# Performance work log

Measured on AMD Instinct MI355X. Metric: run time of the kernel, lower is better.

The kernel has to match this reference:

```python
import jax, jax.numpy as jnp
import numpy as np

N_NODES = 400_000
N_EDGES = 1_600_000
F_IN = 100          # len(nonterminals)
EMB = 128           # opts.embedding_dim
SORTK = 64          # opts.sortk
G = 11              # 1 goal graph + 10 local-context graphs (classifier_1 = Linear(11*dense_dim,...))
D_CAT = 3 * EMB + 1 # concat of x1,x2,x3,x4
K5 = 3 * EMB + 1    # conv5 kernel == stride
DENSE_DIM = ((SORTK - 2) // 2 + 1 - 5 + 1) * EMB  # 28*128 = 3584


def setup_inputs() -> dict:
    key = jax.random.key(0)
    ks = jax.random.split(key, 16)
    s = 0.05
    inp = {
        "x": jax.random.normal(ks[0], (N_NODES, F_IN), jnp.float32),
        "edge_index": jax.random.randint(ks[1], (2, N_EDGES), 0, N_NODES, jnp.int64 if jax.config.jax_enable_x64 else jnp.int32),
        "batch": jnp.sort(jax.random.randint(ks[2], (N_NODES,), 0, G)),
        # GCNConv weights (PyG: x @ W + b after propagation)
        "W1": jax.random.normal(ks[3], (F_IN, EMB), jnp.float32) * s,
        "b1": jnp.zeros((EMB,), jnp.float32),
        "W2": jax.random.normal(ks[4], (EMB, EMB), jnp.float32) * s,
        "b2": jnp.zeros((EMB,), jnp.float32),
        "W3": jax.random.normal(ks[5], (EMB, EMB), jnp.float32) * s,
        "b3": jnp.zeros((EMB,), jnp.float32),
        "W4": jax.random.normal(ks[6], (EMB, 1), jnp.float32) * s,
        "b4": jnp.zeros((1,), jnp.float32),
        # Conv1d(1, EMB//2, K5, stride=K5)
        "cw5": jax.random.normal(ks[7], (EMB // 2, 1, K5), jnp.float32) * s,
        "cb5": jnp.zeros((EMB // 2,), jnp.float32),
        # Conv1d(EMB//2, EMB, 5, stride=1)
        "cw6": jax.random.normal(ks[8], (EMB, EMB // 2, 5), jnp.float32) * s,
        "cb6": jnp.zeros((EMB,), jnp.float32),
        # Linear(11*dense_dim, 128), Linear(128, 10)
        "fw1": jax.random.normal(ks[9], (128, G * DENSE_DIM), jnp.float32) * s,
        "fb1": jnp.zeros((128,), jnp.float32),
        "fw2": jax.random.normal(ks[10], (10, 128), jnp.float32) * s,
        "fb2": jnp.zeros((10,), jnp.float32),
    }
    return inp


def _gcn(x, W, b, src, dst, norm, self_norm):
    # GCNConv: h = x W; out_i = sum_{j->i} norm_ji * h_j + self_norm_i * h_i + b
    h = x @ W
    agg = jax.ops.segment_sum(h[src] * norm[:, None], dst, num_segments=x.shape[0])
    return agg + h * self_norm[:, None] + b


def _conv1d(x, w, b, stride):
    # x: [G, C_in, L], w: [C_out, C_in, K]
    out = jax.lax.conv_general_dilated(x, w, (stride,), 'VALID',
                                       dimension_numbers=('NCH', 'OIH', 'NCH'))
    return out + b[None, :, None]


def reference(x, edge_index, batch, W1, b1, W2, b2, W3, b3, W4, b4,
              cw5, cb5, cw6, cb6, fw1, fb1, fw2, fb2):
    N = x.shape[0]
    src, dst = edge_index[0], edge_index[1]
    # remove_self_loops, then GCNConv re-adds normalized self loops
    keep = (src != dst).astype(x.dtype)
    deg = jax.ops.segment_sum(keep, dst, num_segments=N) + 1.0  # +1 for self loop
    dis = jax.lax.rsqrt(deg)
    norm = dis[src] * dis[dst] * keep          # per-edge sym norm (0 for self loops)
    self_norm = dis * dis                       # deg^{-1} for the added self loop

    x1 = jnp.tanh(_gcn(x, W1, b1, src, dst, norm, self_norm))
    x2 = jnp.tanh(_gcn(x1, W2, b2, src, dst, norm, self_norm))
    x3 = jnp.tanh(_gcn(x2, W3, b3, src, dst, norm, self_norm))
    x4 = jnp.tanh(_gcn(x3, W4, b4, src, dst, norm, self_norm))
    xc = jnp.concatenate([x1, x2, x3, x4], axis=-1)  # [N, 385]

    # global_sort_pool: per-graph sort by last channel (descending), take top-k, zero-pad
    score = xc[:, -1]
    order = jnp.lexsort((-score, batch))  # primary: batch, secondary: -score
    b_sorted = batch[order]
    f_sorted = xc[order]
    counts = jax.ops.segment_sum(jnp.ones_like(batch), batch, num_segments=G)
    starts = jnp.concatenate([jnp.zeros((1,), counts.dtype), jnp.cumsum(counts)[:-1]])
    rank = jnp.arange(N) - starts[b_sorted]
    pooled = jnp.zeros((G, SORTK, D_CAT), xc.dtype).at[b_sorted, rank].set(
        f_sorted, mode='drop')  # ranks >= SORTK dropped
    pooled = pooled.reshape(G, 1, SORTK * D_CAT)  # [G, 1, k*D]

    h = jax.nn.relu(_conv1d(pooled, cw5, cb5, K5))       # [G, EMB//2, SORTK]
    Lh = h.shape[-1]
    h = h.reshape(G, EMB // 2, Lh // 2, 2).max(axis=-1)   # MaxPool1d(2,2)
    h = jax.nn.relu(_conv1d(h, cw6, cb6, 1))              # [G, EMB, L-4]
    emb = h.reshape(-1)  # flatten all 11 graphs -> [11*dense_dim]

    out = jax.nn.relu(emb @ fw1.T + fb1)
    logits = out @ fw2.T + fb2  # dropout is identity at eval
    return logits[None, :]      # logits.view(-1, len(logits)) -> [1, 10]
```

## Files before the change

kernel.cpp:

```cpp
#include <hip/hip_runtime.h>
#include <hip/hip_bf16.h>


#define NN 400000
#define EE 1600000
#define GG 11
#define DCAT 385
#define CCAP 40960

__device__ __forceinline__ float us2f(unsigned short u) {
    return __uint_as_float(((unsigned)u) << 16);
}
__device__ __forceinline__ float ldf(const void* p, long i, int dt) {
    return dt ? ((const float*)p)[i] : us2f(((const unsigned short*)p)[i]);
}
__device__ __forceinline__ unsigned fkey(float s) {
    unsigned u = __float_as_uint(s);
    return (u & 0x80000000u) ? ~u : (u | 0x80000000u);
}

__global__ void k_detect(const unsigned int* __restrict__ xw, int* __restrict__ flag) {
    if (threadIdx.x == 0) {
        int good = 0;
        for (int i = 0; i < 64; ++i) {
            float a = fabsf(us2f((unsigned short)(xw[i] & 0xffffu)));
            if (a > 0.004f && a < 16.f) ++good;
        }
        *flag = (good >= 32) ? 0 : 1;
    }
}

__global__ void k_deg(const int* __restrict__ ei, int* __restrict__ degcnt) {
    int e = blockIdx.x * 256 + threadIdx.x;
    if (e >= EE) return;
    int s = ei[e], d = ei[EE + e];
    if (s != d) atomicAdd(&degcnt[d], 1);
}

__global__ void k_dis(const int* __restrict__ degcnt, float* __restrict__ dis) {
    int i = blockIdx.x * 256 + threadIdx.x;
    if (i < NN) dis[i] = 1.0f / sqrtf((float)degcnt[i] + 1.0f);
}

__global__ __launch_bounds__(256) void k_scan1(const int* __restrict__ in,
                                               int* __restrict__ out1,
                                               int* __restrict__ bsums, int n) {
    __shared__ int lds[256];
    int tid = threadIdx.x;
    int base = blockIdx.x * 1024 + tid * 4;
    int v0 = (base + 0 < n) ? in[base + 0] : 0;
    int v1 = (base + 1 < n) ? in[base + 1] : 0;
    int v2 = (base + 2 < n) ? in[base + 2] : 0;
    int v3 = (base + 3 < n) ? in[base + 3] : 0;
    v1 += v0; v2 += v1; v3 += v2;
    lds[tid] = v3;
    __syncthreads();
    for (int off = 1; off < 256; off <<= 1) {
        int x = (tid >= off) ? lds[tid - off] : 0;
        __syncthreads();
        lds[tid] += x;
        __syncthreads();
    }
    int prefix = (tid > 0) ? lds[tid - 1] : 0;
    if (base + 0 < n) out1[base + 0] = prefix + v0;
    if (base + 1 < n) out1[base + 1] = prefix + v1;
    if (base + 2 < n) out1[base + 2] = prefix + v2;
    if (base + 3 < n) out1[base + 3] = prefix + v3;
    if (tid == 255) bsums[blockIdx.x] = lds[255];
}

__global__ __launch_bounds__(512) void k_scan2(int* __restrict__ bsums, int nb) {
    __shared__ int lds[512];
    int tid = threadIdx.x;
    lds[tid] = (tid < nb) ? bsums[tid] : 0;
    __syncthreads();
    for (int off = 1; off < 512; off <<= 1) {
        int x = (tid >= off) ? lds[tid - off] : 0;
        __syncthreads();
        lds[tid] += x;
        __syncthreads();
    }
    int ex = (tid > 0) ? lds[tid - 1] : 0;
    if (tid < nb) bsums[tid] = ex;
}

__global__ void k_scan3(int* __restrict__ rowptr, const int* __restrict__ bsums, int n) {
    int i = blockIdx.x * 256 + threadIdx.x;
    if (i < n) rowptr[i + 1] += bsums[i >> 10];
    if (i == 0) rowptr[0] = 0;
}

__global__ void k_fill(const int* __restrict__ ei, const int* __restrict__ rowptr,
                       int* __restrict__ fill, int* __restrict__ col) {
    int e = blockIdx.x * 256 + threadIdx.x;
    if (e >= EE) return;
    int s = ei[e], d = ei[EE + e];
    if (s != d) {
        int p = atomicAdd(&fill[d], 1);
        col[rowptr[d] + p] = s;
    }
}

__global__ __launch_bounds__(256, 2) void k_mm1(const void* __restrict__ Xin_,
                                                const void* __restrict__ W,
                                                const int* __restrict__ flag,
                                                float* __restrict__ H) {
    __shared__ float wlds[100 * 128];
    const int dt = *flag;
    const int tid = threadIdx.x;
    if (dt) {
        const float* Wf = (const float*)W;
        for (int idx = tid; idx < 100 * 128; idx += 256) wlds[idx] = Wf[idx];
    } else {
        const unsigned short* Wb = (const unsigned short*)W;
        for (int idx = tid; idx < 100 * 128; idx += 256) wlds[idx] = us2f(Wb[idx]);
    }
    __syncthreads();
    const int tx = tid & 15, ty = tid >> 4;
    const int c0 = tx * 8;
    const size_t r0 = (size_t)blockIdx.x * 64 + (size_t)ty * 4;
    float acc[4][8];
#pragma unroll
    for (int i = 0; i < 4; i++)
#pragma unroll
        for (int c = 0; c < 8; c++) acc[i][c] = 0.f;

    for (int k = 0; k < 100; k += 4) {
        float a[4][4];
        if (dt) {
#pragma unroll
            for (int i = 0; i < 4; i++) {
                const float* p = (const float*)Xin_ + (r0 + i) * 100 + k;
                float4 f = *(const float4*)p;
                a[i][0] = f.x; a[i][1] = f.y; a[i][2] = f.z; a[i][3] = f.w;
            }
        } else {
#pragma unroll
            for (int i = 0; i < 4; i++) {
                const unsigned short* p = (const unsigned short*)Xin_ + (r0 + i) * 100 + k;
                ushort4 u = *(const ushort4*)p;
                a[i][0] = us2f(u.x); a[i][1] = us2f(u.y);
                a[i][2] = us2f(u.z); a[i][3] = us2f(u.w);
            }
        }
#pragma unroll
        for (int j = 0; j < 4; j++) {
            float4 b01 = *(const float4*)&wlds[(k + j) * 128 + c0];
            float4 b23 = *(const float4*)&wlds[(k + j) * 128 + c0 + 4];
            float bb[8] = {b01.x, b01.y, b01.z, b01.w, b23.x, b23.y, b23.z, b23.w};
#pragma unroll
            for (int i = 0; i < 4; i++)
#pragma unroll
                for (int c = 0; c < 8; c++)
                    acc[i][c] = fmaf(a[i][j], bb[c], acc[i][c]);
        }
    }
#pragma unroll
    for (int i = 0; i < 4; i++) {
        float4 o0 = {acc[i][0], acc[i][1], acc[i][2], acc[i][3]};
        float4 o1 = {acc[i][4], acc[i][5], acc[i][6], acc[i][7]};
        *(float4*)&H[(r0 + i) * 128 + c0] = o0;
        *(float4*)&H[(r0 + i) * 128 + c0 + 4] = o1;
    }
}

__global__ __launch_bounds__(256, 2) void k_mm(const float* __restrict__ Xin,
                                               const void* __restrict__ W,
                                               const int* __restrict__ flag,
                                               float* __restrict__ H) {
    __shared__ float wlds[128 * 128];
    const int dt = *flag;
    const int tid = threadIdx.x;
    if (dt) {
        const float* Wf = (const float*)W;
        for (int idx = tid; idx < 128 * 128; idx += 256) wlds[idx] = Wf[idx];
    } else {
        const unsigned short* Wb = (const unsigned short*)W;
        for (int idx = tid; idx < 128 * 128; idx += 256) wlds[idx] = us2f(Wb[idx]);
    }
    __syncthreads();
    const int tx = tid & 15, ty = tid >> 4;
    const int c0 = tx * 8;
    const size_t r0 = (size_t)blockIdx.x * 64 + (size_t)ty * 4;
    float acc[4][8];
#pragma unroll
    for (int i = 0; i < 4; i++)
#pragma unroll
        for (int c = 0; c < 8; c++) acc[i][c] = 0.f;

    for (int k = 0; k < 128; k += 4) {
        float a[4][4];
#pragma unroll
        for (int i = 0; i < 4; i++) {
            float4 f = *(const float4*)&Xin[(r0 + i) * 128 + k];
            a[i][0] = f.x; a[i][1] = f.y; a[i][2] = f.z; a[i][3] = f.w;
        }
#pragma unroll
        for (int j = 0; j < 4; j++) {
            float4 b01 = *(const float4*)&wlds[(k + j) * 128 + c0];
            float4 b23 = *(const float4*)&wlds[(k + j) * 128 + c0 + 4];
            float bb[8] = {b01.x, b01.y, b01.z, b01.w, b23.x, b23.y, b23.z, b23.w};
#pragma unroll
            for (int i = 0; i < 4; i++)
#pragma unroll
                for (int c = 0; c < 8; c++)
                    acc[i][c] = fmaf(a[i][j], bb[c], acc[i][c]);
        }
    }
#pragma unroll
    for (int i = 0; i < 4; i++) {
        float4 o0 = {acc[i][0], acc[i][1], acc[i][2], acc[i][3]};
        float4 o1 = {acc[i][4], acc[i][5], acc[i][6], acc[i][7]};
        *(float4*)&H[(r0 + i) * 128 + c0] = o0;
        *(float4*)&H[(r0 + i) * 128 + c0 + 4] = o1;
    }
}

__global__ __launch_bounds__(256) void k_agg(const float* __restrict__ H,
                                             const float* __restrict__ dis,
                                             const int* __restrict__ rowptr,
                                             const int* __restrict__ col,
                                             const void* __restrict__ bias,
                                             const int* __restrict__ flag,
                                             float* __restrict__ Xout) {
    const int dt = *flag;
    const int lane = threadIdx.x & 31;
    const int node = blockIdx.x * 8 + (threadIdx.x >> 5);
    if (node >= NN) return;
    const int c0 = lane * 4;
    const size_t base = (size_t)node * 128 + c0;
    float4 h = *(const float4*)&H[base];
    float sn = dis[node], s2 = sn * sn;
    float4 acc;
    acc.x = fmaf(h.x, s2, ldf(bias, c0 + 0, dt));
    acc.y = fmaf(h.y, s2, ldf(bias, c0 + 1, dt));
    acc.z = fmaf(h.z, s2, ldf(bias, c0 + 2, dt));
    acc.w = fmaf(h.w, s2, ldf(bias, c0 + 3, dt));
    int e1 = rowptr[node + 1];
    for (int e = rowptr[node]; e < e1; ++e) {
        int nb = col[e];
        float w = dis[nb] * sn;
        float4 hn = *(const float4*)&H[(size_t)nb * 128 + c0];
        acc.x = fmaf(hn.x, w, acc.x);
        acc.y = fmaf(hn.y, w, acc.y);
        acc.z = fmaf(hn.z, w, acc.z);
        acc.w = fmaf(hn.w, w, acc.w);
    }
    float4 o = {tanhf(acc.x), tanhf(acc.y), tanhf(acc.z), tanhf(acc.w)};
    *(float4*)&Xout[base] = o;
}

__global__ __launch_bounds__(256) void k_h4(const float* __restrict__ H3,
                                            const float* __restrict__ dis,
                                            const int* __restrict__ rowptr,
                                            const int* __restrict__ col,
                                            const void* __restrict__ b3,
                                            const void* __restrict__ W4,
                                            const int* __restrict__ flag,
                                            float* __restrict__ h4) {
    const int dt = *flag;
    const int lane = threadIdx.x & 31;
    const int node = blockIdx.x * 8 + (threadIdx.x >> 5);
    if (node >= NN) return;
    const int c0 = lane * 4;
    const size_t base = (size_t)node * 128 + c0;
    float4 h = *(const float4*)&H3[base];
    float sn = dis[node], s2 = sn * sn;
    float4 acc;
    acc.x = fmaf(h.x, s2, ldf(b3, c0 + 0, dt));
    acc.y = fmaf(h.y, s2, ldf(b3, c0 + 1, dt));
    acc.z = fmaf(h.z, s2, ldf(b3, c0 + 2, dt));
    acc.w = fmaf(h.w, s2, ldf(b3, c0 + 3, dt));
    int e1 = rowptr[node + 1];
    for (int e = rowptr[node]; e < e1; ++e) {
        int nb = col[e];
        float w = dis[nb] * sn;
        float4 hn = *(const float4*)&H3[(size_t)nb * 128 + c0];
        acc.x = fmaf(hn.x, w, acc.x);
        acc.y = fmaf(hn.y, w, acc.y);
        acc.z = fmaf(hn.z, w, acc.z);
        acc.w = fmaf(hn.w, w, acc.w);
    }
    float v = tanhf(acc.x) * ldf(W4, c0 + 0, dt) + tanhf(acc.y) * ldf(W4, c0 + 1, dt) +
              tanhf(acc.z) * ldf(W4, c0 + 2, dt) + tanhf(acc.w) * ldf(W4, c0 + 3, dt);
#pragma unroll
    for (int off = 16; off > 0; off >>= 1) v += __shfl_xor(v, off, 64);
    if (lane == 0) h4[node] = v;
}

__global__ void k_agg4(const float* __restrict__ h4, const float* __restrict__ dis,
                       const int* __restrict__ rowptr, const int* __restrict__ col,
                       const void* __restrict__ b4, const int* __restrict__ flag,
                       float* __restrict__ score) {
    const int dt = *flag;
    int i = blockIdx.x * 256 + threadIdx.x;
    if (i >= NN) return;
    float sn = dis[i];
    float acc = fmaf(h4[i] * sn, sn, ldf(b4, 0, dt));
    int e1 = rowptr[i + 1];
    for (int e = rowptr[i]; e < e1; ++e) {
        int nb = col[e];
        acc = fmaf(h4[nb] * dis[nb], sn, acc);
    }
    score[i] = tanhf(acc);
}

__global__ void k_hist(const float* __restrict__ score, const int* __restrict__ batch,
                       int* __restrict__ hist) {
    int i = blockIdx.x * 256 + threadIdx.x;
    if (i >= NN) return;
    unsigned u = fkey(score[i]);
    atomicAdd(&hist[batch[i] * 2048 + (u >> 21)], 1);
}

__global__ void k_thr(const int* __restrict__ hist, int* __restrict__ thr) {
    int g = threadIdx.x;
    if (g < GG) {
        int cum = 0, b = 0;
        for (int bin = 2047; bin >= 0; --bin) {
            cum += hist[g * 2048 + bin];
            if (cum >= 64) { b = bin; break; }
        }
        thr[g] = b;
    }
}

__global__ void k_collect(const float* __restrict__ score, const int* __restrict__ batch,
                          const int* __restrict__ thr, int* __restrict__ ccnt,
                          unsigned long long* __restrict__ cbuf) {
    int i = blockIdx.x * 256 + threadIdx.x;
    if (i >= NN) return;
    int g = batch[i];
    unsigned u = fkey(score[i]);
    if ((int)(u >> 21) >= thr[g]) {
        int p = atomicAdd(&ccnt[g], 1);
        if (p < CCAP)
            cbuf[(size_t)g * CCAP + p] =
                ((unsigned long long)u << 32) | (unsigned)(~(unsigned)i);
    }
}

__global__ __launch_bounds__(64) void k_top64(const unsigned long long* __restrict__ cbuf,
                                              const int* __restrict__ ccnt,
                                              int* __restrict__ sel) {
    __shared__ unsigned long long lds[4096];
    int g = blockIdx.x, t = threadIdx.x;
    int C = ccnt[g];
    if (C > CCAP) C = CCAP;
    const unsigned long long* src = cbuf + (size_t)g * CCAP;
    int CL = C < 4096 ? C : 4096;
    for (int i = t; i < CL; i += 64) lds[i] = src[i];
    __syncthreads();
    unsigned long long prev = ~0ULL;
    for (int k = 0; k < 64; ++k) {
        unsigned long long best = 0;
        for (int i = t; i < CL; i += 64) {
            unsigned long long v = lds[i];
            if (v < prev && v > best) best = v;
        }
        for (int i = 4096 + t; i < C; i += 64) {
            unsigned long long v = src[i];
            if (v < prev && v > best) best = v;
        }
#pragma unroll
        for (int off = 32; off > 0; off >>= 1) {
            unsigned long long o = __shfl_xor(best, off, 64);
            if (o > best) best = o;
        }
        if (t == 0)
            sel[g * 64 + k] = (best == 0) ? -1 : (int)~(unsigned)(best & 0xffffffffu);
        prev = best;
    }
}

__global__ __launch_bounds__(128) void k_x1sel(const void* __restrict__ x,
                                               const void* __restrict__ W1,
                                               const void* __restrict__ b1,
                                               const float* __restrict__ dis,
                                               const int* __restrict__ rowptr,
                                               const int* __restrict__ col,
                                               const int* __restrict__ sel,
                                               const int* __restrict__ flag,
                                               float* __restrict__ X1sel) {
    __shared__ float wl[100 * 128];
    __shared__ float xr[104];
    const int dt = *flag;
    int p = blockIdx.x, t = threadIdx.x;
    if (dt) {
        const float* Wf = (const float*)W1;
        for (int idx = t; idx < 100 * 128; idx += 128) wl[idx] = Wf[idx];
    } else {
        const unsigned short* Wb = (const unsigned short*)W1;
        for (int idx = t; idx < 100 * 128; idx += 128) wl[idx] = us2f(Wb[idx]);
    }
    int si = sel[p];
    __syncthreads();
    if (si < 0) { X1sel[p * 128 + t] = 0.f; return; }
    float sn = dis[si], s2 = sn * sn;
    for (int idx = t; idx < 100; idx += 128) xr[idx] = ldf(x, (long)si * 100 + idx, dt);
    __syncthreads();
    float h = 0.f;
    for (int k = 0; k < 100; ++k) h = fmaf(xr[k], wl[k * 128 + t], h);
    float acc = fmaf(h, s2, ldf(b1, t, dt));
    int e0 = rowptr[si], e1 = rowptr[si + 1];
    for (int e = e0; e < e1; ++e) {
        int nb = col[e];
        __syncthreads();
        for (int idx = t; idx < 100; idx += 128) xr[idx] = ldf(x, (long)nb * 100 + idx, dt);
        __syncthreads();
        h = 0.f;
        for (int k = 0; k < 100; ++k) h = fmaf(xr[k], wl[k * 128 + t], h);
        acc = fmaf(h, dis[nb] * sn, acc);
    }
    X1sel[p * 128 + t] = tanhf(acc);
}

__global__ __launch_bounds__(128) void k_x3sel(const float* __restrict__ H3,
                                               const void* __restrict__ b3,
                                               const float* __restrict__ dis,
                                               const int* __restrict__ rowptr,
                                               const int* __restrict__ col,
                                               const int* __restrict__ sel,
                                               const int* __restrict__ flag,
                                               float* __restrict__ X3sel) {
    const int dt = *flag;
    int p = blockIdx.x, t = threadIdx.x;
    int si = sel[p];
    if (si < 0) { X3sel[p * 128 + t] = 0.f; return; }
    float sn = dis[si], s2 = sn * sn;
    float acc = fmaf(H3[(size_t)si * 128 + t], s2, ldf(b3, t, dt));
    int e1 = rowptr[si + 1];
    for (int e = rowptr[si]; e < e1; ++e) {
        int nb = col[e];
        acc = fmaf(H3[(size_t)nb * 128 + t], dis[nb] * sn, acc);
    }
    X3sel[p * 128 + t] = tanhf(acc);
}

__global__ __launch_bounds__(64) void k_gconv5(const int* __restrict__ sel,
                                               const float* __restrict__ X1sel,
                                               const float* __restrict__ X2,
                                               const float* __restrict__ X3sel,
                                               const float* __restrict__ score,
                                               const void* __restrict__ cw5,
                                               const void* __restrict__ cb5,
                                               const int* __restrict__ flag,
                                               float* __restrict__ h5) {
    __shared__ float feat[DCAT];
    const int dt = *flag;
    int g = blockIdx.x >> 6, t = blockIdx.x & 63;
    int p = g * 64 + t;
    int si = sel[p];
    for (int d = threadIdx.x; d < DCAT; d += 64) {
        float v = 0.f;
        if (si >= 0) {
            if (d < 128) v = X1sel[p * 128 + d];
            else if (d < 256) v = X2[(size_t)si * 128 + d - 128];
            else if (d < 384) v = X3sel[p * 128 + d - 256];
            else v = score[si];
        }
        feat[d] = v;
    }
    __syncthreads();
    int oc = threadIdx.x;
    float acc = ldf(cb5, oc, dt);
    if (dt) {
        const float* w = (const float*)cw5 + (size_t)oc * DCAT;
        for (int d = 0; d < DCAT; ++d) acc = fmaf(feat[d], w[d], acc);
    } else {
        const unsigned short* w = (const unsigned short*)cw5 + (size_t)oc * DCAT;
        for (int d = 0; d < DCAT; ++d) acc = fmaf(feat[d], us2f(w[d]), acc);
    }
    h5[(g * 64 + oc) * 64 + t] = fmaxf(acc, 0.f);
}

__global__ __launch_bounds__(128) void k_conv6(const float* __restrict__ h5,
                                               const void* __restrict__ cw6,
                                               const void* __restrict__ cb6,
                                               const int* __restrict__ flag,
                                               float* __restrict__ emb) {
    __shared__ float hp[64][32];
    const int dt = *flag;
    int g = blockIdx.x;
    for (int idx = threadIdx.x; idx < 2048; idx += 128) {
        int ic = idx >> 5, u = idx & 31;
        float a = h5[g * 4096 + ic * 64 + 2 * u];
        float b = h5[g * 4096 + ic * 64 + 2 * u + 1];
        hp[ic][u] = fmaxf(a, b);
    }
    __syncthreads();
    int oc = threadIdx.x;
    float acc[28];
#pragma unroll
    for (int p = 0; p < 28; ++p) acc[p] = 0.f;
    for (int ic = 0; ic < 64; ++ic) {
        float w[5];
#pragma unroll
        for (int k = 0; k < 5; ++k) w[k] = ldf(cw6, (long)oc * 320 + ic * 5 + k, dt);
        float hv[32];
#pragma unroll
        for (int u = 0; u < 32; ++u) hv[u] = hp[ic][u];
#pragma unroll
        for (int p = 0; p < 28; ++p)
#pragma unroll
            for (int k = 0; k < 5; ++k) acc[p] = fmaf(hv[p + k], w[k], acc[p]);
    }
    float cb = ldf(cb6, oc, dt);
    for (int p = 0; p < 28; ++p)
        emb[g * 3584 + oc * 28 + p] = fmaxf(acc[p] + cb, 0.f);
}

__global__ __launch_bounds__(256) void k_fc1(const float* __restrict__ emb,
                                             const void* __restrict__ fw1,
                                             const void* __restrict__ fb1,
                                             const int* __restrict__ flag,
                                             float* __restrict__ out128) {
    __shared__ float red[256];
    const int dt = *flag;
    int j = blockIdx.x;
    float acc = 0.f;
    if (dt) {
        const float* w = (const float*)fw1 + (size_t)j * 39424;
        for (int i = threadIdx.x; i < 39424; i += 256) acc = fmaf(emb[i], w[i], acc);
    } else {
        const unsigned short* w = (const unsigned short*)fw1 + (size_t)j * 39424;
        for (int i = threadIdx.x; i < 39424; i += 256) acc = fmaf(emb[i], us2f(w[i]), acc);
    }
    red[threadIdx.x] = acc;
    __syncthreads();
    for (int s = 128; s > 0; s >>= 1) {
        if (threadIdx.x < s) red[threadIdx.x] += red[threadIdx.x + s];
        __syncthreads();
    }
    if (threadIdx.x == 0) out128[j] = fmaxf(red[0] + ldf(fb1, j, dt), 0.f);
}

__global__ void k_fc2(const float* __restrict__ out128,
                      const void* __restrict__ fw2,
                      const void* __restrict__ fb2,
                      const int* __restrict__ flag,
                      void* __restrict__ outv) {
    const int dt = *flag;
    int c = threadIdx.x;
    if (c < 10) {
        float acc = ldf(fb2, c, dt);
        for (int j = 0; j < 128; ++j) acc = fmaf(out128[j], ldf(fw2, c * 128 + j, dt), acc);
        if (dt) ((float*)outv)[c] = acc;
        else ((__hip_bfloat16*)outv)[c] = __float2bfloat16(acc);
    }
}

__global__ void k_zero_out(void* outv, int n, const int* flag) {
    const int dt = *flag;
    int i = threadIdx.x;
    if (i < n) {
        if (dt) ((float*)outv)[i] = 0.f;
        else ((__hip_bfloat16*)outv)[i] = __float2bfloat16(0.f);
    }
}

extern "C" void kernel_launch(void* const* d_in, const int* in_sizes, int n_in,
                              void* d_out, int out_size, void* d_ws, size_t ws_size,
                              hipStream_t stream) {
    const void* x = d_in[0];
    const int* ei = (const int*)d_in[1];
    const int* batch = (const int*)d_in[2];
    const void* W1 = d_in[3];
    const void* b1 = d_in[4];
    const void* W2 = d_in[5];
    const void* b2 = d_in[6];
    const void* W3 = d_in[7];
    const void* b3 = d_in[8];
    const void* W4 = d_in[9];
    const void* b4 = d_in[10];
    const void* cw5 = d_in[11];
    const void* cb5 = d_in[12];
    const void* cw6 = d_in[13];
    const void* cb6 = d_in[14];
    const void* fw1 = d_in[15];
    const void* fb1 = d_in[16];
    const void* fw2 = d_in[17];
    const void* fb2 = d_in[18];

    int* i_flag = (int*)d_ws;
    const size_t BIG = (size_t)NN * 128;
    float* f_A = (float*)d_ws + 4;
    float* f_B = f_A + BIG;
    float* f_dis = f_B + BIG;
    float* f_score = f_dis + NN;
    float* f_h4 = f_score + NN;
    float* f_h5 = f_h4 + NN;
    float* f_emb = f_h5 + 45056;
    float* f_o128 = f_emb + 39424;
    float* f_X1sel = f_o128 + 128;
    float* f_X3sel = f_X1sel + 704 * 128;
    int* i_degcnt = (int*)(f_X3sel + 704 * 128);
    int* i_fill = i_degcnt + NN;
    int* i_hist = i_fill + NN;
    int* i_ccnt = i_hist + GG * 2048;
    int* i_rowptr = i_ccnt + 16;
    int* i_col = i_rowptr + NN + 1;
    int* i_bsum = i_col + EE;
    int* i_thr = i_bsum + 512;
    int* i_sel = i_thr + 16;
    unsigned long long* c_buf =
        (unsigned long long*)(((size_t)(i_sel + 704) + 15) & ~(size_t)15);
    size_t need_bytes = (size_t)((char*)(c_buf + (size_t)GG * CCAP) - (char*)d_ws);

    if (ws_size < 64) return;
    k_detect<<<1, 64, 0, stream>>>((const unsigned int*)x, i_flag);

    if (ws_size < need_bytes) {
        k_zero_out<<<1, 64, 0, stream>>>(d_out, out_size, i_flag);
        return;
    }

    const int EB = (EE + 255) / 256;
    const int NB = (NN + 255) / 256;
    const int SB = (NN + 1023) / 1024;

    hipMemsetAsync(i_degcnt, 0, sizeof(int) * (2 * NN + GG * 2048 + 16), stream);

    k_deg<<<EB, 256, 0, stream>>>(ei, i_degcnt);
    k_dis<<<NB, 256, 0, stream>>>(i_degcnt, f_dis);
    k_scan1<<<SB, 256, 0, stream>>>(i_degcnt, i_rowptr + 1, i_bsum, NN);
    k_scan2<<<1, 512, 0, stream>>>(i_bsum, SB);
    k_scan3<<<NB, 256, 0, stream>>>(i_rowptr, i_bsum, NN);
    k_fill<<<EB, 256, 0, stream>>>(ei, i_rowptr, i_fill, i_col);

    const int MMB = NN / 64;
    const int AGB = NN / 8;

    k_mm1<<<MMB, 256, 0, stream>>>(x, W1, i_flag, f_A);
    k_agg<<<AGB, 256, 0, stream>>>(f_A, f_dis, i_rowptr, i_col, b1, i_flag, f_B);
    k_mm<<<MMB, 256, 0, stream>>>(f_B, W2, i_flag, f_A);
    k_agg<<<AGB, 256, 0, stream>>>(f_A, f_dis, i_rowptr, i_col, b2, i_flag, f_B);
    k_mm<<<MMB, 256, 0, stream>>>(f_B, W3, i_flag, f_A);
    k_h4<<<AGB, 256, 0, stream>>>(f_A, f_dis, i_rowptr, i_col, b3, W4, i_flag, f_h4);
    k_agg4<<<NB, 256, 0, stream>>>(f_h4, f_dis, i_rowptr, i_col, b4, i_flag, f_score);

    k_hist<<<NB, 256, 0, stream>>>(f_score, batch, i_hist);
    k_thr<<<1, 64, 0, stream>>>(i_hist, i_thr);
    k_collect<<<NB, 256, 0, stream>>>(f_score, batch, i_thr, i_ccnt, c_buf);
    k_top64<<<GG, 64, 0, stream>>>(c_buf, i_ccnt, i_sel);

    k_x1sel<<<GG * 64, 128, 0, stream>>>(x, W1, b1, f_dis, i_rowptr, i_col, i_sel, i_flag, f_X1sel);
    k_x3sel<<<GG * 64, 128, 0, stream>>>(f_A, b3, f_dis, i_rowptr, i_col, i_sel, i_flag, f_X3sel);

    k_gconv5<<<GG * 64, 64, 0, stream>>>(i_sel, f_X1sel, f_B, f_X3sel, f_score, cw5, cb5, i_flag, f_h5);
    k_conv6<<<GG, 128, 0, stream>>>(f_h5, cw6, cb6, i_flag, f_emb);
    k_fc1<<<128, 256, 0, stream>>>(f_emb, fw1, fb1, i_flag, f_o128);
    k_fc2<<<1, 128, 0, stream>>>(f_o128, fw2, fb2, i_flag, d_out);

    (void)in_sizes; (void)n_in; (void)ws_size;
}
```

Before: 2.085 ms.

## Enlarge GEMM register tile to 8x8 and unroll neighbor gathers by four

The dense node-feature matmuls now give each thread 8 rows instead of 4. Columns are split into two strided groups of four (c0 and c0+64), and each block covers 128 rows, which halves the grid. This is meant to raise FMA work per LDS load and reduce LDS bank conflicts, at the cost of more accumulator registers. The CSR aggregation loops in k_agg, k_h4 and k_agg4 are unrolled by four so several independent neighbor loads are in flight before the FMAs. In k_agg4 this also changes the floating-point summation order.

```diff
diff --git a/kernel.cpp b/kernel.cpp
--- a/kernel.cpp
+++ b/kernel.cpp
@@ -101,6 +101,28 @@
     }
 }
 
+__device__ __forceinline__ void mm_inner(const float (&a)[8][4],
+                                         const float* __restrict__ wlds, int k,
+                                         int c0, float (&acc)[8][8]) {
+#pragma unroll
+    for (int j = 0; j < 4; j++) {
+        float4 b0 = *(const float4*)&wlds[(k + j) * 128 + c0];
+        float4 b1 = *(const float4*)&wlds[(k + j) * 128 + c0 + 64];
+#pragma unroll
+        for (int i = 0; i < 8; i++) {
+            float av = a[i][j];
+            acc[i][0] = fmaf(av, b0.x, acc[i][0]);
+            acc[i][1] = fmaf(av, b0.y, acc[i][1]);
+            acc[i][2] = fmaf(av, b0.z, acc[i][2]);
+            acc[i][3] = fmaf(av, b0.w, acc[i][3]);
+            acc[i][4] = fmaf(av, b1.x, acc[i][4]);
+            acc[i][5] = fmaf(av, b1.y, acc[i][5]);
+            acc[i][6] = fmaf(av, b1.z, acc[i][6]);
+            acc[i][7] = fmaf(av, b1.w, acc[i][7]);
+        }
+    }
+}
+
 __global__ __launch_bounds__(256, 2) void k_mm1(const void* __restrict__ Xin_,
                                                 const void* __restrict__ W,
                                                 const int* __restrict__ flag,
@@ -117,50 +139,42 @@
     }
     __syncthreads();
     const int tx = tid & 15, ty = tid >> 4;
-    const int c0 = tx * 8;
-    const size_t r0 = (size_t)blockIdx.x * 64 + (size_t)ty * 4;
-    float acc[4][8];
-#pragma unroll
-    for (int i = 0; i < 4; i++)
+    const int c0 = tx * 4;
+    const size_t r0 = (size_t)blockIdx.x * 128 + (size_t)ty * 8;
+    float acc[8][8];
+#pragma unroll
+    for (int i = 0; i < 8; i++)
 #pragma unroll
         for (int c = 0; c < 8; c++) acc[i][c] = 0.f;
 
-    for (int k = 0; k < 100; k += 4) {
-        float a[4][4];
-        if (dt) {
-#pragma unroll
-            for (int i = 0; i < 4; i++) {
-                const float* p = (const float*)Xin_ + (r0 + i) * 100 + k;
-                float4 f = *(const float4*)p;
+    if (dt) {
+        for (int k = 0; k < 100; k += 4) {
+            float a[8][4];
+#pragma unroll
+            for (int i = 0; i < 8; i++) {
+                float4 f = *(const float4*)((const float*)Xin_ + (r0 + i) * 100 + k);
                 a[i][0] = f.x; a[i][1] = f.y; a[i][2] = f.z; a[i][3] = f.w;
             }
-        } else {
-#pragma unroll
-            for (int i = 0; i < 4; i++) {
-                const unsigned short* p = (const unsigned short*)Xin_ + (r0 + i) * 100 + k;
-                ushort4 u = *(const ushort4*)p;
+            mm_inner(a, wlds, k, c0, acc);
+        }
+    } else {
+        for (int k = 0; k < 100; k += 4) {
+            float a[8][4];
+#pragma unroll
+            for (int i = 0; i < 8; i++) {
+                ushort4 u = *(const ushort4*)((const unsigned short*)Xin_ + (r0 + i) * 100 + k);
                 a[i][0] = us2f(u.x); a[i][1] = us2f(u.y);
                 a[i][2] = us2f(u.z); a[i][3] = us2f(u.w);
             }
-        }
-#pragma unroll
-        for (int j = 0; j < 4; j++) {
-            float4 b01 = *(const float4*)&wlds[(k + j) * 128 + c0];
-            float4 b23 = *(const float4*)&wlds[(k + j) * 128 + c0 + 4];
-            float bb[8] = {b01.x, b01.y, b01.z, b01.w, b23.x, b23.y, b23.z, b23.w};
-#pragma unroll
-            for (int i = 0; i < 4; i++)
-#pragma unroll
-                for (int c = 0; c < 8; c++)
-                    acc[i][c] = fmaf(a[i][j], bb[c], acc[i][c]);
-        }
-    }
-#pragma unroll
-    for (int i = 0; i < 4; i++) {
+            mm_inner(a, wlds, k, c0, acc);
+        }
+    }
+#pragma unroll
+    for (int i = 0; i < 8; i++) {
         float4 o0 = {acc[i][0], acc[i][1], acc[i][2], acc[i][3]};
         float4 o1 = {acc[i][4], acc[i][5], acc[i][6], acc[i][7]};
         *(float4*)&H[(r0 + i) * 128 + c0] = o0;
-        *(float4*)&H[(r0 + i) * 128 + c0 + 4] = o1;
+        *(float4*)&H[(r0 + i) * 128 + c0 + 64] = o1;
     }
 }
 
@@ -180,39 +194,29 @@
     }
     __syncthreads();
     const int tx = tid & 15, ty = tid >> 4;
-    const int c0 = tx * 8;
-    const size_t r0 = (size_t)blockIdx.x * 64 + (size_t)ty * 4;
-    float acc[4][8];
-#pragma unroll
-    for (int i = 0; i < 4; i++)
+    const int c0 = tx * 4;
+    const size_t r0 = (size_t)blockIdx.x * 128 + (size_t)ty * 8;
+    float acc[8][8];
+#pragma unroll
+    for (int i = 0; i < 8; i++)
 #pragma unroll
         for (int c = 0; c < 8; c++) acc[i][c] = 0.f;
 
     for (int k = 0; k < 128; k += 4) {
-        float a[4][4];
-#pragma unroll
-        for (int i = 0; i < 4; i++) {
+        float a[8][4];
+#pragma unroll
+        for (int i = 0; i < 8; i++) {
             float4 f = *(const float4*)&Xin[(r0 + i) * 128 + k];
             a[i][0] = f.x; a[i][1] = f.y; a[i][2] = f.z; a[i][3] = f.w;
         }
-#pragma unroll
-        for (int j = 0; j < 4; j++) {
-            float4 b01 = *(const float4*)&wlds[(k + j) * 128 + c0];
-            float4 b23 = *(const float4*)&wlds[(k + j) * 128 + c0 + 4];
-            float bb[8] = {b01.x, b01.y, b01.z, b01.w, b23.x, b23.y, b23.z, b23.w};
-#pragma unroll
-            for (int i = 0; i < 4; i++)
-#pragma unroll
-                for (int c = 0; c < 8; c++)
-                    acc[i][c] = fmaf(a[i][j], bb[c], acc[i][c]);
-        }
-    }
-#pragma unroll
-    for (int i = 0; i < 4; i++) {
+        mm_inner(a, wlds, k, c0, acc);
+    }
+#pragma unroll
+    for (int i = 0; i < 8; i++) {
         float4 o0 = {acc[i][0], acc[i][1], acc[i][2], acc[i][3]};
         float4 o1 = {acc[i][4], acc[i][5], acc[i][6], acc[i][7]};
         *(float4*)&H[(r0 + i) * 128 + c0] = o0;
-        *(float4*)&H[(r0 + i) * 128 + c0 + 4] = o1;
+        *(float4*)&H[(r0 + i) * 128 + c0 + 64] = o1;
     }
 }
 
@@ -236,15 +240,29 @@
     acc.y = fmaf(h.y, s2, ldf(bias, c0 + 1, dt));
     acc.z = fmaf(h.z, s2, ldf(bias, c0 + 2, dt));
     acc.w = fmaf(h.w, s2, ldf(bias, c0 + 3, dt));
-    int e1 = rowptr[node + 1];
-    for (int e = rowptr[node]; e < e1; ++e) {
+    int e = rowptr[node], e1 = rowptr[node + 1];
+    for (; e + 4 <= e1; e += 4) {
+        int n0 = col[e], n1 = col[e + 1], n2 = col[e + 2], n3 = col[e + 3];
+        float w0 = dis[n0] * sn, w1 = dis[n1] * sn, w2 = dis[n2] * sn, w3 = dis[n3] * sn;
+        float4 h0 = *(const float4*)&H[(size_t)n0 * 128 + c0];
+        float4 h1 = *(const float4*)&H[(size_t)n1 * 128 + c0];
+        float4 h2 = *(const float4*)&H[(size_t)n2 * 128 + c0];
+        float4 h3 = *(const float4*)&H[(size_t)n3 * 128 + c0];
+        acc.x = fmaf(h0.x, w0, acc.x); acc.y = fmaf(h0.y, w0, acc.y);
+        acc.z = fmaf(h0.z, w0, acc.z); acc.w = fmaf(h0.w, w0, acc.w);
+        acc.x = fmaf(h1.x, w1, acc.x); acc.y = fmaf(h1.y, w1, acc.y);
+        acc.z = fmaf(h1.z, w1, acc.z); acc.w = fmaf(h1.w, w1, acc.w);
+        acc.x = fmaf(h2.x, w2, acc.x); acc.y = fmaf(h2.y, w2, acc.y);
+        acc.z = fmaf(h2.z, w2, acc.z); acc.w = fmaf(h2.w, w2, acc.w);
+        acc.x = fmaf(h3.x, w3, acc.x); acc.y = fmaf(h3.y, w3, acc.y);
+        acc.z = fmaf(h3.z, w3, acc.z); acc.w = fmaf(h3.w, w3, acc.w);
+    }
+    for (; e < e1; ++e) {
         int nb = col[e];
         float w = dis[nb] * sn;
         float4 hn = *(const float4*)&H[(size_t)nb * 128 + c0];
-        acc.x = fmaf(hn.x, w, acc.x);
-        acc.y = fmaf(hn.y, w, acc.y);
-        acc.z = fmaf(hn.z, w, acc.z);
-        acc.w = fmaf(hn.w, w, acc.w);
+        acc.x = fmaf(hn.x, w, acc.x); acc.y = fmaf(hn.y, w, acc.y);
+        acc.z = fmaf(hn.z, w, acc.z); acc.w = fmaf(hn.w, w, acc.w);
     }
     float4 o = {tanhf(acc.x), tanhf(acc.y), tanhf(acc.z), tanhf(acc.w)};
     *(float4*)&Xout[base] = o;
@@ -271,15 +289,29 @@
     acc.y = fmaf(h.y, s2, ldf(b3, c0 + 1, dt));
     acc.z = fmaf(h.z, s2, ldf(b3, c0 + 2, dt));
     acc.w = fmaf(h.w, s2, ldf(b3, c0 + 3, dt));
-    int e1 = rowptr[node + 1];
-    for (int e = rowptr[node]; e < e1; ++e) {
+    int e = rowptr[node], e1 = rowptr[node + 1];
+    for (; e + 4 <= e1; e += 4) {
+        int n0 = col[e], n1 = col[e + 1], n2 = col[e + 2], n3 = col[e + 3];
+        float w0 = dis[n0] * sn, w1 = dis[n1] * sn, w2 = dis[n2] * sn, w3 = dis[n3] * sn;
+        float4 h0 = *(const float4*)&H3[(size_t)n0 * 128 + c0];
+        float4 h1 = *(const float4*)&H3[(size_t)n1 * 128 + c0];
+        float4 h2 = *(const float4*)&H3[(size_t)n2 * 128 + c0];
+        float4 h3 = *(const float4*)&H3[(size_t)n3 * 128 + c0];
+        acc.x = fmaf(h0.x, w0, acc.x); acc.y = fmaf(h0.y, w0, acc.y);
+        acc.z = fmaf(h0.z, w0, acc.z); acc.w = fmaf(h0.w, w0, acc.w);
+        acc.x = fmaf(h1.x, w1, acc.x); acc.y = fmaf(h1.y, w1, acc.y);
+        acc.z = fmaf(h1.z, w1, acc.z); acc.w = fmaf(h1.w, w1, acc.w);
+        acc.x = fmaf(h2.x, w2, acc.x); acc.y = fmaf(h2.y, w2, acc.y);
+        acc.z = fmaf(h2.z, w2, acc.z); acc.w = fmaf(h2.w, w2, acc.w);
+        acc.x = fmaf(h3.x, w3, acc.x); acc.y = fmaf(h3.y, w3, acc.y);
+        acc.z = fmaf(h3.z, w3, acc.z); acc.w = fmaf(h3.w, w3, acc.w);
+    }
+    for (; e < e1; ++e) {
         int nb = col[e];
         float w = dis[nb] * sn;
         float4 hn = *(const float4*)&H3[(size_t)nb * 128 + c0];
-        acc.x = fmaf(hn.x, w, acc.x);
-        acc.y = fmaf(hn.y, w, acc.y);
-        acc.z = fmaf(hn.z, w, acc.z);
-        acc.w = fmaf(hn.w, w, acc.w);
+        acc.x = fmaf(hn.x, w, acc.x); acc.y = fmaf(hn.y, w, acc.y);
+        acc.z = fmaf(hn.z, w, acc.z); acc.w = fmaf(hn.w, w, acc.w);
     }
     float v = tanhf(acc.x) * ldf(W4, c0 + 0, dt) + tanhf(acc.y) * ldf(W4, c0 + 1, dt) +
               tanhf(acc.z) * ldf(W4, c0 + 2, dt) + tanhf(acc.w) * ldf(W4, c0 + 3, dt);
@@ -297,8 +329,14 @@
     if (i >= NN) return;
     float sn = dis[i];
     float acc = fmaf(h4[i] * sn, sn, ldf(b4, 0, dt));
-    int e1 = rowptr[i + 1];
-    for (int e = rowptr[i]; e < e1; ++e) {
+    int e = rowptr[i], e1 = rowptr[i + 1];
+    for (; e + 4 <= e1; e += 4) {
+        int n0 = col[e], n1 = col[e + 1], n2 = col[e + 2], n3 = col[e + 3];
+        float v0 = h4[n0] * dis[n0], v1 = h4[n1] * dis[n1];
+        float v2 = h4[n2] * dis[n2], v3 = h4[n3] * dis[n3];
+        acc = fmaf(v0 + v1 + v2 + v3, sn, acc);
+    }
+    for (; e < e1; ++e) {
         int nb = col[e];
         acc = fmaf(h4[nb] * dis[nb], sn, acc);
     }
@@ -628,7 +666,7 @@
     k_scan3<<<NB, 256, 0, stream>>>(i_rowptr, i_bsum, NN);
     k_fill<<<EB, 256, 0, stream>>>(ei, i_rowptr, i_fill, i_col);
 
-    const int MMB = NN / 64;
+    const int MMB = NN / 128;
     const int AGB = NN / 8;
 
     k_mm1<<<MMB, 256, 0, stream>>>(x, W1, i_flag, f_A);
```

Result: faster. 1.920 ms (-7.9%).
